# Kernel tuning notes

Hardware: AMD Instinct MI355X
Metric: run time of the kernel (lower is better)

## Reference

```python
import jax, jax.numpy as jnp
import numpy as np
import math

IMAGE_SIZE = 300
STEPS = [16, 32, 64, 100, 150, 300]
MIN_SIZES = [60, 105, 150, 195, 240, 285]
MAX_SIZES = [105, 150, 195, 240, 285, 330]
ASPECT_RATIOS = [2, 3]
SCORE_THRESH = 0.02
NMS_THRESH = 0.45
POST_NMS_TOP_N = 100
VAR_XY, VAR_WH = 0.1, 0.2
BATCH, NUM_CLASSES = 16, 201


def _make_priors():
    # SSD-style anchor generation in (cx, cy, w, h), relative coords.
    priors = []
    for k, step in enumerate(STEPS):
        f = math.ceil(IMAGE_SIZE / step)
        s = MIN_SIZES[k] / IMAGE_SIZE
        sp = math.sqrt(MIN_SIZES[k] * MAX_SIZES[k]) / IMAGE_SIZE
        for i in range(f):
            for j in range(f):
                cx = (j + 0.5) * step / IMAGE_SIZE
                cy = (i + 0.5) * step / IMAGE_SIZE
                priors.append([cx, cy, s, s])
                priors.append([cx, cy, sp, sp])
                for ar in ASPECT_RATIOS:
                    r = math.sqrt(ar)
                    priors.append([cx, cy, s * r, s / r])
                    priors.append([cx, cy, s / r, s * r])
    return np.asarray(priors, dtype=np.float32)  # [3000, 4]


def setup_inputs() -> dict:
    key = jax.random.key(0)
    k1, k2 = jax.random.split(key)
    priors = jnp.asarray(_make_priors())  # [P, 4]
    P = priors.shape[0]
    pred_bbox_deltas = jax.random.normal(k1, (BATCH, P, 4), dtype=jnp.float32)
    objectness = jax.random.normal(k2, (BATCH, P, NUM_CLASSES), dtype=jnp.float32)
    return {"pred_bbox_deltas": pred_bbox_deltas, "objectness": objectness, "priors": priors}


def reference(pred_bbox_deltas, objectness, priors):
    # Eval path of MultiBoxHeads.filter_priors: softmax -> box decode ->
    # score filter -> class-aware (batched) NMS -> top-N, padded to fixed size.
    P = priors.shape[0]
    C = objectness.shape[-1]
    probs = jax.nn.softmax(objectness, axis=-1)  # [B, P, C]

    # BoxCoder.decode with variances (0.1, 0.2); priors are (cx, cy, w, h).
    pxy, pwh = priors[:, :2], priors[:, 2:]
    xy = pred_bbox_deltas[..., :2] * VAR_XY * pwh + pxy  # [B, P, 2]
    wh = jnp.exp(pred_bbox_deltas[..., 2:] * VAR_WH) * pwh
    decoded = jnp.concatenate([xy - 0.5 * wh, xy + 0.5 * wh], axis=-1)  # [B, P, 4] xyxy

    # Per-candidate class labels (background class 0 dropped), shared across images.
    labels = jnp.broadcast_to(jnp.arange(1, C), (P, C - 1)).reshape(-1)  # [P*(C-1)] int

    def nms_image(dec, prob):
        scores = prob[:, 1:].reshape(-1)  # [P*(C-1)]
        boxes = jnp.broadcast_to(dec[:, None, :], (P, C - 1, 4)).reshape(-1, 4)
        s = jnp.where(scores > SCORE_THRESH, scores, -1.0)
        # batched_nms trick: offset boxes by label so classes never overlap.
        off = jnp.max(boxes) + 1.0
        bo = boxes + labels.astype(boxes.dtype)[:, None] * off
        areas = (bo[:, 2] - bo[:, 0]) * (bo[:, 3] - bo[:, 1])

        def step(s, _):
            i = jnp.argmax(s)
            sc = s[i]
            b = bo[i]
            ix1 = jnp.maximum(bo[:, 0], b[0])
            iy1 = jnp.maximum(bo[:, 1], b[1])
            ix2 = jnp.minimum(bo[:, 2], b[2])
            iy2 = jnp.minimum(bo[:, 3], b[3])
            inter = jnp.clip(ix2 - ix1, 0.0) * jnp.clip(iy2 - iy1, 0.0)
            iou = inter / (areas + areas[i] - inter)
            s = jnp.where(iou > NMS_THRESH, -1.0, s).at[i].set(-1.0)
            return s, (i, sc)

        _, (idx, sc) = jax.lax.scan(step, s, None, length=POST_NMS_TOP_N)
        ok = sc > SCORE_THRESH  # slots that hold real detections
        b_out = jnp.where(ok[:, None], jnp.clip(boxes[idx], 0.0, 1.0), 0.0)  # parse() clamp
        s_out = jnp.where(ok, sc, 0.0)
        l_out = jnp.where(ok, labels[idx].astype(boxes.dtype), 0.0)
        # [K, 6] = (x1, y1, x2, y2, score, label); zero rows are padding.
        return jnp.concatenate([b_out, s_out[:, None], l_out[:, None]], axis=-1)

    return jax.vmap(nms_image)(decoded, probs)  # [B, POST_NMS_TOP_N, 6]
```

## Files before the change

kernel.cpp:

```cpp
#include <hip/hip_runtime.h>
#include <cfloat>
#include <cstdint>

#define BATCH 16
#define PRIORS 3000
#define NCLS 201
#define NLBL 200
#define TOPN 100
#define SCORE_THR 0.02f
#define NMS_THR 0.45f

#define FPPB 16
#define FBLK ((PRIORS + FPPB - 1) / FPPB)
#define SEGW 64
#define SEGS (FBLK * 4)
#define SLOTS (SEGS * SEGW)
#define HOTW 8
#define OVF_CAP 1024
#define T0 0.08f

#define NMS_T 1024
#define NBINS 1024
#define HCAP 512
#define SB_BASE 0x3CA3

__device__ __forceinline__ int key_stratum(uint64_t k) {
    int s = (int)(k >> 48) - SB_BASE;
    return s < 0 ? 0 : (s > NBINS - 1 ? NBINS - 1 : s);
}

__global__ __launch_bounds__(256) void score_filter_kernel(
    const float* __restrict__ obj,
    int*         __restrict__ cnt,
    int*         __restrict__ hcnt,
    uint64_t*    __restrict__ seg,
    uint64_t*    __restrict__ hot,
    uint64_t*    __restrict__ ovf,
    uint64_t*    __restrict__ hovf)
{
    const int b    = blockIdx.y;
    const int wave = threadIdx.x >> 6;
    const int lane = threadIdx.x & 63;
    const int segId = blockIdx.x * 4 + wave;
    uint64_t* myseg = seg + ((size_t)b * SEGS + segId) * SEGW;
    uint64_t* myhot = hot + ((size_t)b * SEGS + segId) * HOTW;
    const int pbase = blockIdx.x * FPPB + wave * 4;

    float v0[4], v1[4], v2[4], v3[4];
    bool pv[4];
#pragma unroll
    for (int pp = 0; pp < 4; ++pp) {
        int p = pbase + pp;
        pv[pp] = (p < PRIORS);
        const float* x = obj + ((size_t)b * PRIORS + (pv[pp] ? p : PRIORS - 1)) * NCLS;
        v0[pp] = x[lane];
        v1[pp] = x[lane + 64];
        v2[pp] = x[lane + 128];
        v3[pp] = (lane + 192 < NCLS) ? x[lane + 192] : -FLT_MAX;
    }
    float mx[4];
#pragma unroll
    for (int pp = 0; pp < 4; ++pp)
        mx[pp] = fmaxf(fmaxf(v0[pp], v1[pp]), fmaxf(v2[pp], v3[pp]));
    for (int d = 32; d > 0; d >>= 1) {
#pragma unroll
        for (int pp = 0; pp < 4; ++pp)
            mx[pp] = fmaxf(mx[pp], __shfl_xor(mx[pp], d, 64));
    }
    float e0[4], e1[4], e2[4], e3[4], se[4];
#pragma unroll
    for (int pp = 0; pp < 4; ++pp) {
        e0[pp] = expf(v0[pp] - mx[pp]);
        e1[pp] = expf(v1[pp] - mx[pp]);
        e2[pp] = expf(v2[pp] - mx[pp]);
        e3[pp] = (lane + 192 < NCLS) ? expf(v3[pp] - mx[pp]) : 0.0f;
        se[pp] = e0[pp] + e1[pp] + e2[pp] + e3[pp];
    }
    for (int d = 32; d > 0; d >>= 1) {
#pragma unroll
        for (int pp = 0; pp < 4; ++pp)
            se[pp] += __shfl_xor(se[pp], d, 64);
    }
    int cursor = 0, hcur = 0;
#pragma unroll
    for (int pp = 0; pp < 4; ++pp) {
        float inv = 1.0f / se[pp];
        int p = pbase + pp;
        float ev[4] = { e0[pp], e1[pp], e2[pp], e3[pp] };
#pragma unroll
        for (int k = 0; k < 4; ++k) {
            int c = lane + 64 * k;
            float prob = ev[k] * inv;
            bool pass = pv[pp] && (c >= 1) && (c < NCLS) && (prob > SCORE_THR);
            uint64_t mask = __ballot(pass);
            bool hotp = pass && (prob > T0);
            uint64_t hmask = __ballot(hotp);
            if (pass) {
                uint32_t oid = (uint32_t)(p * NLBL + (c - 1));
                uint64_t key = ((uint64_t)__float_as_uint(prob) << 32)
                             | (uint64_t)(0xFFFFFFFFu - oid);
                int idx = cursor + __popcll(mask & ((1ull << lane) - 1ull));
                if (idx < SEGW) {
                    myseg[idx] = key;
                } else {
                    int gi = atomicAdd(&cnt[b], 1);
                    if (gi < OVF_CAP) ovf[(size_t)b * OVF_CAP + gi] = key;
                }
                if (hotp) {
                    int hidx = hcur + __popcll(hmask & ((1ull << lane) - 1ull));
                    if (hidx < HOTW) {
                        myhot[hidx] = key;
                    } else {
                        int gi = atomicAdd(&hcnt[b], 1);
                        if (gi < OVF_CAP) hovf[(size_t)b * OVF_CAP + gi] = key;
                    }
                }
            }
            cursor += (int)__popcll(mask);
            hcur   += (int)__popcll(hmask);
        }
    }
    if (lane >= (cursor < SEGW ? cursor : SEGW)) myseg[lane] = 0ull;
    if (lane < HOTW && lane >= (hcur < HOTW ? hcur : HOTW)) myhot[lane] = 0ull;
}

__device__ __forceinline__ void sort512_desc(const uint64_t* skey,
                                             uint64_t K[8], int lane)
{
#pragma unroll
    for (int r = 0; r < 8; ++r) K[r] = skey[r * 64 + lane];
#pragma unroll
    for (int k2 = 2; k2 <= 512; k2 <<= 1) {
#pragma unroll
        for (int j2 = k2 >> 1; j2 >= 64; j2 >>= 1) {
            int j2r = j2 >> 6;
#pragma unroll
            for (int r = 0; r < 8; ++r) {
                if ((r & j2r) == 0) {
                    int rp = r | j2r;
                    bool up = ((((r << 6) + lane) & k2) == 0);
                    uint64_t a = K[r], bb = K[rp];
                    uint64_t mxk = a > bb ? a : bb;
                    uint64_t mnk = a > bb ? bb : a;
                    K[r]  = up ? mxk : mnk;
                    K[rp] = up ? mnk : mxk;
                }
            }
        }
#pragma unroll
        for (int j2 = ((k2 >> 1) < 32 ? (k2 >> 1) : 32); j2 >= 1; j2 >>= 1) {
#pragma unroll
            for (int r = 0; r < 8; ++r) {
                uint64_t o = __shfl_xor((unsigned long long)K[r], j2, 64);
                bool up = ((((r << 6) + lane) & k2) == 0);
                bool lower = ((lane & j2) == 0);
                K[r] = (up == lower) ? (K[r] > o ? K[r] : o)
                                     : (K[r] < o ? K[r] : o);
            }
        }
    }
}

__device__ __forceinline__ int scan_sorted_w0(
    const uint64_t K[8], int b, const float4* __restrict__ dbox, float ofb,
    float4* abox, float* aarea, int na, float* __restrict__ out, int lane)
{
#pragma unroll
    for (int r = 0; r < 8; ++r) {
        if (na >= TOPN) break;
        uint64_t myk = K[r];
        bool valid = (myk != 0ull);
        uint32_t oid = 0xFFFFFFFFu - (uint32_t)myk;
        int p = valid ? (int)(oid / NLBL) : 0;
        int c = valid ? ((int)(oid - (uint32_t)p * NLBL) + 1) : 1;
        float4 db = dbox[p];
        float lof = (float)c * ofb;
        float qx1 = db.x + lof, qy1 = db.y + lof;
        float qx2 = db.z + lof, qy2 = db.w + lof;
        float aq = (qx2 - qx1) * (qy2 - qy1);
        bool dead = false;
        for (int l = 0; l < na; ++l) {
            float4 a = abox[l];
            float ix1 = fmaxf(qx1, a.x), iy1 = fmaxf(qy1, a.y);
            float ix2 = fminf(qx2, a.z), iy2 = fminf(qy2, a.w);
            float inter = fmaxf(ix2 - ix1, 0.0f) * fmaxf(iy2 - iy1, 0.0f);
            float iou = inter / (aq + aarea[l] - inter);
            if (iou > NMS_THR) dead = true;
        }
        uint64_t alive = __ballot(valid && !dead);
        while (alive != 0ull && na < TOPN) {
            int j = __ffsll((unsigned long long)alive) - 1;
            float ax1 = __shfl(qx1, j, 64);
            float ay1 = __shfl(qy1, j, 64);
            float ax2 = __shfl(qx2, j, 64);
            float ay2 = __shfl(qy2, j, 64);
            float aa  = __shfl(aq,  j, 64);
            if (lane == j) {
                abox[na]  = make_float4(qx1, qy1, qx2, qy2);
                aarea[na] = aq;
                float* o = out + ((size_t)b * TOPN + na) * 6;
                o[0] = fminf(fmaxf(db.x, 0.0f), 1.0f);
                o[1] = fminf(fmaxf(db.y, 0.0f), 1.0f);
                o[2] = fminf(fmaxf(db.z, 0.0f), 1.0f);
                o[3] = fminf(fmaxf(db.w, 0.0f), 1.0f);
                o[4] = __uint_as_float((uint32_t)(myk >> 32));
                o[5] = (float)c;
            }
            na++;
            bool mine = ((alive >> lane) & 1ull) != 0ull;
            bool drop = (lane == j);
            if (mine && !drop) {
                float ix1 = fmaxf(qx1, ax1), iy1 = fmaxf(qy1, ay1);
                float ix2 = fminf(qx2, ax2), iy2 = fminf(qy2, ay2);
                float inter = fmaxf(ix2 - ix1, 0.0f) * fmaxf(iy2 - iy1, 0.0f);
                float iou = inter / (aq + aa - inter);
                if (iou > NMS_THR) drop = true;
            }
            alive = __ballot(mine && !drop);
        }
    }
    return na;
}

__device__ __forceinline__ int scan_step_w0(
    uint64_t key, int b, const float4* __restrict__ dbox, float ofb,
    float4* abox, float* aarea, int na, float* __restrict__ out, int lane)
{
    uint32_t oid = 0xFFFFFFFFu - (uint32_t)key;
    int p = (int)(oid / NLBL);
    int c = (int)(oid - (uint32_t)p * NLBL) + 1;
    float4 db = dbox[p];
    float lo = (float)c * ofb;
    float qx1 = db.x + lo, qy1 = db.y + lo;
    float qx2 = db.z + lo, qy2 = db.w + lo;
    float aq = (qx2 - qx1) * (qy2 - qy1);
    bool sup = false;
    for (int l = lane; l < na; l += 64) {
        float4 a = abox[l];
        float ix1 = fmaxf(qx1, a.x), iy1 = fmaxf(qy1, a.y);
        float ix2 = fminf(qx2, a.z), iy2 = fminf(qy2, a.w);
        float inter = fmaxf(ix2 - ix1, 0.0f) * fmaxf(iy2 - iy1, 0.0f);
        float iou = inter / (aq + aarea[l] - inter);
        if (iou > NMS_THR) sup = true;
    }
    if (__ballot(sup) == 0ull) {
        if (lane == 0) {
            abox[na]  = make_float4(qx1, qy1, qx2, qy2);
            aarea[na] = aq;
            float* o = out + ((size_t)b * TOPN + na) * 6;
            o[0] = fminf(fmaxf(db.x, 0.0f), 1.0f);
            o[1] = fminf(fmaxf(db.y, 0.0f), 1.0f);
            o[2] = fminf(fmaxf(db.z, 0.0f), 1.0f);
            o[3] = fminf(fmaxf(db.w, 0.0f), 1.0f);
            o[4] = __uint_as_float((uint32_t)(key >> 32));
            o[5] = (float)c;
        }
        __threadfence_block();
        return na + 1;
    }
    return na;
}

__global__ __launch_bounds__(NMS_T) void nms_kernel(
    const float*    __restrict__ deltas,
    const float*    __restrict__ priors,
    const int*      __restrict__ cnt,
    const int*      __restrict__ hcnt,
    const uint64_t* __restrict__ seg,
    const uint64_t* __restrict__ hot,
    const uint64_t* __restrict__ ovf,
    const uint64_t* __restrict__ hovf,
    float*          __restrict__ out)
{
    __shared__ float4   dbox[PRIORS];
    __shared__ int      sufx[NBINS];
    __shared__ uint64_t skey[HCAP];
    __shared__ float4   abox[112];
    __shared__ float    aarea[112];
    __shared__ uint64_t rk[NMS_T / 64];
    __shared__ float    wredF[NMS_T / 64];
    __shared__ int      wtotS[NMS_T / 64];
    __shared__ int      carryS[NMS_T / 64];
    __shared__ int cntC, loS, naS;
    __shared__ uint64_t fkS;

    const int b    = blockIdx.x;
    const int tid  = threadIdx.x;
    const int wave = tid >> 6;
    const int lane = tid & 63;
    const uint64_t* slots  = seg  + (size_t)b * SLOTS;
    const uint64_t* hslots = hot  + (size_t)b * SEGS * HOTW;
    int n_ovf  = cnt[b];  if (n_ovf  > OVF_CAP) n_ovf  = OVF_CAP;
    int n_hovf = hcnt[b]; if (n_hovf > OVF_CAP) n_hovf = OVF_CAP;
    const uint64_t* ovfp  = ovf  + (size_t)b * OVF_CAP;
    const uint64_t* hovfp = hovf + (size_t)b * OVF_CAP;

    if (tid == 0) { cntC = 0; naS = 0; }
    if (lane == 0) wredF[wave] = -FLT_MAX;
    __syncthreads();

    for (int j = tid; j < SEGS * HOTW; j += NMS_T) {
        uint64_t k = hslots[j];
        if (k) { int i = atomicAdd(&cntC, 1); if (i < HCAP) skey[i] = k; }
    }
    for (int j = tid; j < n_hovf; j += NMS_T) {
        uint64_t k = hovfp[j];
        if (k) { int i = atomicAdd(&cntC, 1); if (i < HCAP) skey[i] = k; }
    }
    __syncthreads();
    int hc = cntC;
    bool decoded = false;
    if (hc <= HCAP) {
        if (tid < HCAP && tid >= hc) skey[tid] = 0ull;
        __syncthreads();
        if (wave == 0) {
            uint64_t K[8];
            sort512_desc(skey, K, lane);
            __syncthreads();
            float ofb;
            {
                float v = (lane < NMS_T / 64) ? wredF[lane] : -FLT_MAX;
                for (int d = 32; d > 0; d >>= 1) v = fmaxf(v, __shfl_xor(v, d, 64));
                ofb = v + 1.0f;
            }
            int na = scan_sorted_w0(K, b, dbox, ofb, abox, aarea, 0, out, lane);
            if (lane == 0) naS = na;
        } else {
            int base0 = (wave - 1) * 200;
            float lmax = -FLT_MAX;
            for (int p = base0 + lane; p < base0 + 200; p += 64) {
                float4 d4 = ((const float4*)deltas)[(size_t)b * PRIORS + p];
                float4 pr = ((const float4*)priors)[p];
                float cx = d4.x * 0.1f * pr.z + pr.x;
                float cy = d4.y * 0.1f * pr.w + pr.y;
                float w  = expf(d4.z * 0.2f) * pr.z;
                float h  = expf(d4.w * 0.2f) * pr.w;
                float x1 = cx - 0.5f * w, y1 = cy - 0.5f * h;
                float x2 = cx + 0.5f * w, y2 = cy + 0.5f * h;
                dbox[p] = make_float4(x1, y1, x2, y2);
                lmax = fmaxf(lmax, fmaxf(fmaxf(x1, y1), fmaxf(x2, y2)));
            }
            for (int d = 32; d > 0; d >>= 1)
                lmax = fmaxf(lmax, __shfl_xor(lmax, d, 64));
            if (lane == 0) wredF[wave] = lmax;
            __syncthreads();
        }
        decoded = true;
        __syncthreads();
    }

    if (naS < TOPN) {
        if (!decoded) {
            float lmax = -FLT_MAX;
            for (int p = tid; p < PRIORS; p += NMS_T) {
                float4 d4 = ((const float4*)deltas)[(size_t)b * PRIORS + p];
                float4 pr = ((const float4*)priors)[p];
                float cx = d4.x * 0.1f * pr.z + pr.x;
                float cy = d4.y * 0.1f * pr.w + pr.y;
                float w  = expf(d4.z * 0.2f) * pr.z;
                float h  = expf(d4.w * 0.2f) * pr.w;
                float x1 = cx - 0.5f * w, y1 = cy - 0.5f * h;
                float x2 = cx + 0.5f * w, y2 = cy + 0.5f * h;
                dbox[p] = make_float4(x1, y1, x2, y2);
                lmax = fmaxf(lmax, fmaxf(fmaxf(x1, y1), fmaxf(x2, y2)));
            }
            for (int d = 32; d > 0; d >>= 1)
                lmax = fmaxf(lmax, __shfl_xor(lmax, d, 64));
            if (lane == 0) wredF[wave] = lmax;
        }
        sufx[tid] = 0;
        if (tid == 0) naS = 0;
        __syncthreads();
        for (int j = tid; j < SLOTS; j += NMS_T) {
            uint64_t k = slots[j];
            if (k) atomicAdd(&sufx[key_stratum(k)], 1);
        }
        for (int j = tid; j < n_ovf; j += NMS_T) {
            uint64_t k = ovfp[j];
            if (k) atomicAdd(&sufx[key_stratum(k)], 1);
        }
        __syncthreads();
        {
            int v = sufx[64 * wave + lane];
            int s = v;
            for (int d = 1; d < 64; d <<= 1) {
                int t = __shfl_down(s, d, 64);
                if (lane + d < 64) s += t;
            }
            if (lane == 0) wtotS[wave] = s;
            __syncthreads();
            if (wave == 0 && lane < NMS_T / 64) {
                int tv = wtotS[lane];
                int ts = tv;
                for (int d = 1; d < NMS_T / 64; d <<= 1) {
                    int t = __shfl_down(ts, d, 64);
                    if (lane + d < NMS_T / 64) ts += t;
                }
                carryS[lane] = ts - tv;
            }
            __syncthreads();
            sufx[64 * wave + lane] = s + carryS[wave];
        }
        int curHi = NBINS;
        for (;;) {
            __syncthreads();
            int naCur = naS;
            int A = (curHi < NBINS) ? sufx[curHi] : 0;
            int remaining = sufx[0] - A;
            if (naCur >= TOPN || remaining <= 0 || curHi <= 0) break;
            int target = A + HCAP;
            if (tid == 0) { loS = curHi; cntC = 0; }
            __syncthreads();
            if (tid < curHi) {
                if (sufx[tid] <= target && (tid == 0 || sufx[tid - 1] > target))
                    loS = tid;
            }
            __syncthreads();
            int lo = loS;

            if (lo < curHi) {
                for (int j = tid; j < SLOTS; j += NMS_T) {
                    uint64_t k = slots[j];
                    if (k) {
                        int s = key_stratum(k);
                        if (s >= lo && s < curHi) {
                            int i = atomicAdd(&cntC, 1);
                            if (i < HCAP) skey[i] = k;
                        }
                    }
                }
                for (int j = tid; j < n_ovf; j += NMS_T) {
                    uint64_t k = ovfp[j];
                    if (k) {
                        int s = key_stratum(k);
                        if (s >= lo && s < curHi) {
                            int i = atomicAdd(&cntC, 1);
                            if (i < HCAP) skey[i] = k;
                        }
                    }
                }
                __syncthreads();
                if (tid < HCAP && tid >= cntC) skey[tid] = 0ull;
                __syncthreads();
                if (wave == 0) {
                    uint64_t K[8];
                    sort512_desc(skey, K, lane);
                    float ofb;
                    {
                        float v = (lane < NMS_T / 64) ? wredF[lane] : -FLT_MAX;
                        for (int d = 32; d > 0; d >>= 1) v = fmaxf(v, __shfl_xor(v, d, 64));
                        ofb = v + 1.0f;
                    }
                    int na = scan_sorted_w0(K, b, dbox, ofb, abox, aarea, naS, out, lane);
                    if (lane == 0) naS = na;
                }
                curHi = lo;
            } else {
                float ofbT;
                {
                    float v = (lane < NMS_T / 64) ? wredF[lane] : -FLT_MAX;
                    for (int d = 32; d > 0; d >>= 1) v = fmaxf(v, __shfl_xor(v, d, 64));
                    ofbT = v + 1.0f;
                }
                int s = curHi - 1;
                uint64_t lastK = ~0ull;
                for (;;) {
                    __syncthreads();
                    if (naS >= TOPN) break;
                    uint64_t bk = 0ull;
                    for (int j = tid; j < SLOTS; j += NMS_T) {
                        uint64_t k = slots[j];
                        if (k && key_stratum(k) == s && k < lastK && k > bk) bk = k;
                    }
                    for (int j = tid; j < n_ovf; j += NMS_T) {
                        uint64_t k = ovfp[j];
                        if (k && key_stratum(k) == s && k < lastK && k > bk) bk = k;
                    }
                    for (int d = 32; d > 0; d >>= 1) {
                        uint64_t o = __shfl_xor((unsigned long long)bk, d, 64);
                        bk = (o > bk) ? o : bk;
                    }
                    if (lane == 0) rk[wave] = bk;
                    __syncthreads();
                    if (tid == 0) {
                        uint64_t fk = rk[0];
                        for (int w = 1; w < NMS_T / 64; ++w) fk = (rk[w] > fk) ? rk[w] : fk;
                        fkS = fk;
                    }
                    __syncthreads();
                    uint64_t fk = fkS;
                    if (fk == 0ull) break;
                    if (wave == 0) {
                        int nal = naS;
                        nal = scan_step_w0(fk, b, dbox, ofbT, abox, aarea, nal, out, lane);
                        if (lane == 0) naS = nal;
                    }
                    lastK = fk;
                }
                curHi = s;
            }
        }
    }
    __syncthreads();
    int naF = naS;
    for (int idx = tid; idx < (TOPN - naF) * 6; idx += NMS_T)
        out[(size_t)b * TOPN * 6 + (size_t)naF * 6 + idx] = 0.0f;
}

extern "C" void kernel_launch(void* const* d_in, const int* in_sizes, int n_in,
                              void* d_out, int out_size, void* d_ws, size_t ws_size,
                              hipStream_t stream)
{
    const float* deltas = (const float*)d_in[0];
    const float* obj    = (const float*)d_in[1];
    const float* priors = (const float*)d_in[2];
    float* out = (float*)d_out;

    char* ws = (char*)d_ws;
    int*      cnt  = (int*)ws;
    int*      hcnt = (int*)(ws + 64);
    uint64_t* hotA = (uint64_t*)(ws + 256);
    uint64_t* segA = hotA + (size_t)BATCH * SEGS * HOTW;
    uint64_t* ovfA = segA + (size_t)BATCH * SLOTS;
    uint64_t* hovA = ovfA + (size_t)BATCH * OVF_CAP;

    hipMemsetAsync(ws, 0, 128, stream);
    dim3 fg(FBLK, BATCH, 1);
    score_filter_kernel<<<fg, 256, 0, stream>>>(obj, cnt, hcnt, segA, hotA, ovfA, hovA);
    nms_kernel<<<BATCH, NMS_T, 0, stream>>>(deltas, priors, cnt, hcnt,
                                            segA, hotA, ovfA, hovA, out);
}
```

Baseline: 135.1 us.

## Replace serial greedy NMS scan with parallel IoU bitmask matrix and wave-0 resolve

In the hot-candidate path, the greedy NMS scan that wave 0 ran serially over the sorted keys is replaced. All 1024 threads now build an upper-triangular IoU-over-threshold bitmask matrix for up to 512 sorted candidates in shared memory. Wave 0 then resolves the greedy selection with ballots and bitmask ANDs. This spreads the quadratic IoU work across the whole block but adds about 44KB of shared memory (adj, qbox, qarea), which may hurt occupancy, plus extra barriers.

```diff
diff --git a/kernel.cpp b/kernel.cpp
--- a/kernel.cpp
+++ b/kernel.cpp
@@ -275,6 +275,9 @@
     __shared__ float4   dbox[PRIORS];
     __shared__ int      sufx[NBINS];
     __shared__ uint64_t skey[HCAP];
+    __shared__ float4   qbox[HCAP];
+    __shared__ float    qarea[HCAP];
+    __shared__ uint64_t adj[HCAP * 8];
     __shared__ float4   abox[112];
     __shared__ float    aarea[112];
     __shared__ uint64_t rk[NMS_T / 64];
@@ -316,15 +319,8 @@
         if (wave == 0) {
             uint64_t K[8];
             sort512_desc(skey, K, lane);
-            __syncthreads();
-            float ofb;
-            {
-                float v = (lane < NMS_T / 64) ? wredF[lane] : -FLT_MAX;
-                for (int d = 32; d > 0; d >>= 1) v = fmaxf(v, __shfl_xor(v, d, 64));
-                ofb = v + 1.0f;
-            }
-            int na = scan_sorted_w0(K, b, dbox, ofb, abox, aarea, 0, out, lane);
-            if (lane == 0) naS = na;
+#pragma unroll
+            for (int r = 0; r < 8; ++r) skey[r * 64 + lane] = K[r];
         } else {
             int base0 = (wave - 1) * 200;
             float lmax = -FLT_MAX;
@@ -343,9 +339,88 @@
             for (int d = 32; d > 0; d >>= 1)
                 lmax = fmaxf(lmax, __shfl_xor(lmax, d, 64));
             if (lane == 0) wredF[wave] = lmax;
-            __syncthreads();
         }
         decoded = true;
+        __syncthreads();
+
+        float v = wredF[lane & 15];
+        for (int d = 8; d > 0; d >>= 1) v = fmaxf(v, __shfl_xor(v, d, 64));
+        float ofb = v + 1.0f;
+
+        if (tid < HCAP) {
+            uint64_t k = skey[tid];
+            bool valid = (k != 0ull);
+            uint32_t oid = 0xFFFFFFFFu - (uint32_t)k;
+            int p = valid ? (int)(oid / NLBL) : 0;
+            int c = valid ? ((int)(oid - (uint32_t)p * NLBL) + 1) : 1;
+            float4 db = dbox[p];
+            float lof = (float)c * ofb;
+            float4 q = make_float4(db.x + lof, db.y + lof,
+                                   db.z + lof, db.w + lof);
+            qbox[tid]  = q;
+            qarea[tid] = (q.z - q.x) * (q.w - q.y);
+        }
+        for (int i = tid; i < HCAP * 8; i += NMS_T) adj[i] = 0ull;
+        __syncthreads();
+
+        int hcw = (hc + 63) >> 6;
+        int P2  = (hcw * (hcw + 1)) >> 1;
+        for (int tau = tid; tau < (P2 << 6); tau += NMS_T) {
+            int pair = tau >> 6, rr = tau & 63;
+            int w = 0;
+            while ((((w + 1) * (w + 2)) >> 1) <= pair) ++w;
+            int cw = pair - ((w * (w + 1)) >> 1);
+            int r  = (cw << 6) + rr;
+            float4 qr = qbox[r];
+            float  ar = qarea[r];
+            int jb = w << 6;
+            uint64_t m = 0ull;
+#pragma unroll 8
+            for (int j = 0; j < 64; ++j) {
+                float4 qj = qbox[jb + j];
+                float ix1 = fmaxf(qr.x, qj.x), iy1 = fmaxf(qr.y, qj.y);
+                float ix2 = fminf(qr.z, qj.z), iy2 = fminf(qr.w, qj.w);
+                float inter = fmaxf(ix2 - ix1, 0.0f) * fmaxf(iy2 - iy1, 0.0f);
+                float iou = inter / (ar + qarea[jb + j] - inter);
+                m |= (uint64_t)(iou > NMS_THR) << j;
+            }
+            if (w == cw) m &= ~((1ull << rr) - 1ull);
+            adj[(r << 3) + w] = m;
+        }
+        __syncthreads();
+
+        if (wave == 0) {
+            uint64_t alive = 0ull;
+            if (lane < 8) {
+                int n = hc - (lane << 6);
+                alive = (n >= 64) ? ~0ull : (n > 0 ? ((1ull << n) - 1ull) : 0ull);
+            }
+            int na = 0;
+            while (na < TOPN) {
+                uint64_t nz = __ballot((lane < 8) && (alive != 0ull));
+                if (nz == 0ull) break;
+                int w0 = __ffsll((unsigned long long)nz) - 1;
+                uint64_t aw = (uint64_t)__shfl((long long)alive, w0, 64);
+                int r = (w0 << 6) + __ffsll((unsigned long long)aw) - 1;
+                if (lane < 8) alive &= ~adj[(r << 3) + lane];
+                if (lane == 8) {
+                    uint64_t myk = skey[r];
+                    uint32_t oid = 0xFFFFFFFFu - (uint32_t)myk;
+                    int p = (int)(oid / NLBL);
+                    int c = (int)(oid - (uint32_t)p * NLBL) + 1;
+                    float4 db = dbox[p];
+                    float* o = out + ((size_t)b * TOPN + na) * 6;
+                    o[0] = fminf(fmaxf(db.x, 0.0f), 1.0f);
+                    o[1] = fminf(fmaxf(db.y, 0.0f), 1.0f);
+                    o[2] = fminf(fmaxf(db.z, 0.0f), 1.0f);
+                    o[3] = fminf(fmaxf(db.w, 0.0f), 1.0f);
+                    o[4] = __uint_as_float((uint32_t)(myk >> 32));
+                    o[5] = (float)c;
+                }
+                ++na;
+            }
+            if (lane == 0) naS = na;
+        }
         __syncthreads();
     }
 
```

Measured after the change: 147.5 us. 1.09x slower.
